# Performance work log

Hardware: AMD Instinct MI355X
Metric: run time of the kernel (lower is better)

The kernel has to match this reference:

```python
import jax, jax.numpy as jnp
import numpy as np

EMBED_DIM_LIST = [256, 512]
NUM_HEADS_LIST = [4, 8]
MAX_EMBED = 512
N_BASE = 8                       # = max(num_heads_list)
MAX_HS = max(EMBED_DIM_LIST) // min(NUM_HEADS_LIST)  # 128


def _config_masks():
    # One {0,1} mask per (emb, heads) config, shape [n_cfg, N_BASE, MAX_HS, MAX_EMBED].
    # Mask encodes: slice base weight [:head_size, :emb], zero-pad to (MAX_HS, MAX_EMBED),
    # and that only the first `heads` base heads receive a contribution.
    r = np.arange(MAX_HS)[:, None]
    c = np.arange(MAX_EMBED)[None, :]
    masks = []
    for emb in EMBED_DIM_LIST:
        for heads in NUM_HEADS_LIST:
            hs = emb // heads
            m2 = ((r < hs) & (c < emb)).astype(np.float32)      # [MAX_HS, MAX_EMBED]
            hm = (np.arange(N_BASE) < heads).astype(np.float32)  # [N_BASE]
            masks.append(hm[:, None, None] * m2[None])
    return jnp.asarray(np.stack(masks))  # [4, 8, 128, 512]

_CFG_MASKS = _config_masks()


def setup_inputs() -> dict:
    key = jax.random.key(0)
    k0, k1, k2, k3, k4 = jax.random.split(key, 5)
    B, T = 4, 2048
    x = jax.random.normal(k0, (B, T, MAX_EMBED), dtype=jnp.float32)
    weights = jax.random.uniform(k1, (len(EMBED_DIM_LIST) * len(NUM_HEADS_LIST),), dtype=jnp.float32)
    s = 0.02
    base_K = jax.random.normal(k2, (N_BASE, MAX_HS, MAX_EMBED), dtype=jnp.float32) * s
    base_Q = jax.random.normal(k3, (N_BASE, MAX_HS, MAX_EMBED), dtype=jnp.float32) * s
    base_V = jax.random.normal(k4, (N_BASE, MAX_HS, MAX_EMBED), dtype=jnp.float32) * s
    return {"x": x, "weights": weights, "base_K": base_K, "base_Q": base_Q, "base_V": base_V}


def reference(x, weights, base_K, base_Q, base_V):
    B, T, C = x.shape
    # Weight mixing: sum_i weights[i] * (padded slice of base weight) for each base head.
    eff = jnp.einsum('i,ihde->hde', weights, _CFG_MASKS)  # [H, MAX_HS, MAX_EMBED]
    Wk = eff * base_K
    Wq = eff * base_Q
    Wv = eff * base_V
    # Projections for all base heads at once: F.linear(x, W) == x @ W.T
    k = jnp.einsum('btc,hdc->bhtd', x, Wk)
    q = jnp.einsum('btc,hdc->bhtd', x, Wq)
    v = jnp.einsum('btc,hdc->bhtd', x, Wv)
    # Causal self-attention; scale uses k.shape[-1] == MAX_HS (padded head size), as in source.
    scale = 1.0 / jnp.sqrt(jnp.asarray(MAX_HS, dtype=x.dtype))
    att = jnp.einsum('bhtd,bhsd->bhts', q, k) * scale       # [B, H, T, T]
    tril = jnp.tril(jnp.ones((T, T), dtype=bool))
    att = jnp.where(tril, att, -jnp.inf)
    wei = jax.nn.softmax(att, axis=-1)                       # dropout = identity (eval)
    out = jnp.einsum('bhts,bhsd->bhtd', wei, v)              # [B, H, T, MAX_HS]
    # torch.cat(head_out_list, dim=-1) in head order == transpose + reshape
    return out.transpose(0, 2, 1, 3).reshape(B, T, N_BASE * MAX_HS)
```

## Files before the change

kernel.cpp:

```cpp
#include <hip/hip_runtime.h>
#include <hip/hip_bf16.h>
#include <stdint.h>

typedef __attribute__((ext_vector_type(8))) short bf16x8;
typedef __attribute__((ext_vector_type(4))) float f32x4;
typedef __attribute__((ext_vector_type(16))) float f32x16;

#define MFMA16(a,b,c) __builtin_amdgcn_mfma_f32_16x16x32_bf16((a),(b),(c),0,0,0)
#define MFMA32(a,b,c) __builtin_amdgcn_mfma_f32_32x32x16_bf16((a),(b),(c),0,0,0)
#define AS1 __attribute__((address_space(1)))
#define AS3 __attribute__((address_space(3)))

__device__ inline short f2bf(float f) {
    union { __hip_bfloat16 h; short s; } u;
    u.h = __float2bfloat16(f);
    return u.s;
}
__device__ inline uint32_t pack_bf16(float a, float b) {
    union { __hip_bfloat16 h; uint16_t u; } ua, ub;
    ua.h = __float2bfloat16(a); ub.h = __float2bfloat16(b);
    return (uint32_t)ua.u | ((uint32_t)ub.u << 16);
}

#if __has_builtin(__builtin_amdgcn_permlane32_swap)
#define SWAP32(x, y, a, b) { auto _r = __builtin_amdgcn_permlane32_swap((a),(b),false,false); \
                             (x) = _r[0]; (y) = _r[1]; }
#else
#define SWAP32(x, y, a, b) { uint32_t _ta = __shfl_xor((uint32_t)(a),32); \
                             uint32_t _tb = __shfl_xor((uint32_t)(b),32); \
                             (x) = hh_ ? _tb : (a); (y) = hh_ ? (b) : _ta; }
#endif

#define QSCALE 0.12751879523879295f

#define NW (8*128*512)
#define NX4 (8192*512/4)

__global__ void prep_kernel(const float* __restrict__ x,
                            const float* __restrict__ w,
                            const float* __restrict__ bK,
                            const float* __restrict__ bQ,
                            const float* __restrict__ bV,
                            short* __restrict__ xb,
                            short* __restrict__ W)
{
    const float w0 = w[0], w1 = w[1], w2 = w[2], w3 = w[3];
    for (int i = blockIdx.x * blockDim.x + threadIdx.x; i < NW + NX4;
         i += gridDim.x * blockDim.x) {
        if (i < NW) {
            int e = i & 511;
            int d = (i >> 9) & 127;
            int h = i >> 16;
            float eff = 0.f;
            if (h < 4) { eff += w2; if (d < 64 && e < 256) eff += w0; }
            if (d < 32 && e < 256) eff += w1;
            if (d < 64) eff += w3;
            W[i]          = f2bf(eff * bK[i]);
            W[i + NW]     = f2bf(eff * bQ[i] * QSCALE);
            W[i + 2*NW]   = f2bf(eff * bV[i]);
        } else {
            int j = i - NW;
            float4 v = ((const float4*)x)[j];
            short4 o;
            o.x = f2bf(v.x); o.y = f2bf(v.y); o.z = f2bf(v.z); o.w = f2bf(v.w);
            ((short4*)xb)[j] = o;
        }
    }
}

__global__ __launch_bounds__(256)
void proj_gemm(const short* __restrict__ A,
               const short* __restrict__ Bw,
               short* __restrict__ qkv)
{
    __shared__ short S[128 * 128];
    short* As = S;
    short* Bs = S + 128 * 64;
    const int tid = threadIdx.x;
    const int lane = tid & 63;
    const int wave = tid >> 6;
    const int wr = wave >> 1, wc = wave & 1;
    const int l15 = lane & 15, lk = lane >> 4;

    const int wg = (blockIdx.x & 7) * 192 + (blockIdx.x >> 3);
    const int bm = (wg / 24) * 128;
    const int bn = (wg % 24) * 128;

    char* Ab = (char*)As;
    char* Bb = (char*)Bs;
    char* Sb = (char*)S;
    f32x4 acc[4][4] = {};

    for (int k0 = 0; k0 < 512; k0 += 64) {
        __syncthreads();
#pragma unroll
        for (int i = 0; i < 4; ++i) {
            int c = i * 256 + tid;
            int lin = c * 16;
            int row = lin >> 7;
            int cof = ((lin & 127) ^ ((row & 7) << 4)) >> 1;
            __builtin_amdgcn_global_load_lds(
                (const AS1 void*)(A + (size_t)(bm + row) * 512 + k0 + cof),
                (AS3 void*)(As + c * 8), 16, 0, 0);
            __builtin_amdgcn_global_load_lds(
                (const AS1 void*)(Bw + (size_t)(bn + row) * 512 + k0 + cof),
                (AS3 void*)(Bs + c * 8), 16, 0, 0);
        }
        __syncthreads();
#pragma unroll
        for (int kk = 0; kk < 2; ++kk) {
            bf16x8 af[4], bfv[4];
#pragma unroll
            for (int mi = 0; mi < 4; ++mi) {
                int row = wr * 64 + mi * 16 + l15;
                af[mi] = *(const bf16x8*)(Ab + ((row * 128 + kk * 64 + lk * 16) ^ ((row & 7) << 4)));
            }
#pragma unroll
            for (int ni = 0; ni < 4; ++ni) {
                int row = wc * 64 + ni * 16 + l15;
                bfv[ni] = *(const bf16x8*)(Bb + ((row * 128 + kk * 64 + lk * 16) ^ ((row & 7) << 4)));
            }
#pragma unroll
            for (int mi = 0; mi < 4; ++mi)
#pragma unroll
                for (int ni = 0; ni < 4; ++ni)
                    acc[mi][ni] = MFMA16(af[mi], bfv[ni], acc[mi][ni]);
        }
    }

    const int proj = bn >> 10;
    const int b = bm >> 11;
    const int bh = b * 8 + ((bn & 1023) >> 7);
    const int tbase = bm & 2047;

    __syncthreads();
    if (proj == 2) {
#pragma unroll
        for (int mi = 0; mi < 4; ++mi) {
#pragma unroll
            for (int ni = 0; ni < 4; ++ni) {
                int dl = wc * 64 + ni * 16 + l15;
                int tlb = wr * 64 + mi * 16 + lk * 4;
                int byte0 = (dl * 256 + tlb * 2) ^ ((dl & 7) << 4);
                *(uint32_t*)(Sb + byte0)     = pack_bf16(acc[mi][ni][0], acc[mi][ni][1]);
                *(uint32_t*)(Sb + byte0 + 4) = pack_bf16(acc[mi][ni][2], acc[mi][ni][3]);
            }
        }
    } else {
#pragma unroll
        for (int mi = 0; mi < 4; ++mi) {
#pragma unroll
            for (int ni = 0; ni < 4; ++ni) {
                int dl = wc * 64 + ni * 16 + l15;
#pragma unroll
                for (int r = 0; r < 4; ++r) {
                    int tl = wr * 64 + mi * 16 + lk * 4 + r;
                    *(short*)(Sb + ((tl * 256 + dl * 2) ^ ((tl & 7) << 4))) = f2bf(acc[mi][ni][r]);
                }
            }
        }
    }
    __syncthreads();

    short* dst;
    if (proj == 2)
        dst = qkv + (size_t)2 * (32 * 2048 * 128) + (size_t)bh * 128 * 2048;
    else
        dst = qkv + (size_t)proj * (32 * 2048 * 128) + (size_t)bh * 2048 * 128;

#pragma unroll
    for (int i = 0; i < 8; ++i) {
        int c = i * 256 + tid;
        int row = c >> 4;
        uint4 v = *(const uint4*)(Sb + row * 256 + (((c & 15) * 16) ^ ((row & 7) << 4)));
        if (proj == 2) {
            *(uint4*)(dst + (size_t)row * 2048 + tbase + (c & 15) * 8) = v;
        } else {
            *(uint4*)(dst + (size_t)(tbase + row) * 128 + (c & 15) * 8) = v;
        }
    }
}

__device__ inline void stage_tile(const short* __restrict__ Kp,
                                  const short* __restrict__ Vp,
                                  char* smem, int buf)
{
    short* kls = (short*)(smem + (buf << 14));
    short* vls = (short*)(smem + 32768 + (buf << 14));
    const int tid = threadIdx.x;
#pragma unroll
    for (int i = 0; i < 4; ++i) {
        int c = i * 256 + tid;
        int lin = c * 16;
        int rk = lin >> 8;
        int kof = ((lin & 255) ^ ((rk & 15) << 4)) >> 1;
        __builtin_amdgcn_global_load_lds(
            (const AS1 void*)(Kp + (size_t)rk * 128 + kof),
            (AS3 void*)(kls + c * 8), 16, 0, 0);
        int rv = lin >> 8;
        int p = (lin & 255) ^ ((rv & 15) << 4);
        int d = rv * 2 + (p >> 7);
        int t = (p & 127) >> 1;
        __builtin_amdgcn_global_load_lds(
            (const AS1 void*)(Vp + (size_t)d * 2048 + t),
            (AS3 void*)(vls + c * 8), 16, 0, 0);
    }
}

__global__ __launch_bounds__(256, 2)
void attn_kernel(const short* __restrict__ qkv, float* __restrict__ out)
{
    extern __shared__ char smem[];
    const int tid = threadIdx.x, lane = tid & 63, wave = tid >> 6;
    const int l31 = lane & 31;
    const int hh_ = lane >> 5;

    const int bh = blockIdx.x & 31;
    const int half = blockIdx.x >> 8;
    const int idx = (blockIdx.x >> 5) & 7;
    const int qt = half ? idx : (15 - idx);
    const int q0 = qt * 128;

    const size_t HSTRIDE = (size_t)2048 * 128;
    const short* Kp = qkv + (size_t)bh * HSTRIDE;
    const short* Qp = qkv + (size_t)32 * HSTRIDE + (size_t)bh * HSTRIDE;
    const short* Vp = qkv + (size_t)64 * HSTRIDE + (size_t)bh * 128 * 2048;

    bf16x8 qf[8];
    {
        const short* qrow = Qp + (size_t)(q0 + wave * 32 + l31) * 128 + hh_ * 8;
#pragma unroll
        for (int dblk = 0; dblk < 8; ++dblk)
            qf[dblk] = *(const bf16x8*)(qrow + dblk * 16);
    }

    float mrow = -1e30f, lrow = 0.f;
    f32x16 acco[4] = {};

    const int ntiles = qt * 2 + 2;
    const int qwave = q0 + wave * 32;
    const int qglob = qwave + l31;

    stage_tile(Kp, Vp, smem, 0);
    int cur = 0;

    for (int jt = 0; jt < ntiles; ++jt) {
        const int j0 = jt * 64;
        __builtin_amdgcn_s_barrier();
        if (jt + 1 < ntiles) {
            stage_tile(Kp + (size_t)(j0 + 64) * 128, Vp + (j0 + 64),
                       smem, cur ^ 1);
            asm volatile("s_waitcnt vmcnt(8)" ::: "memory");
        } else {
            asm volatile("s_waitcnt vmcnt(0)" ::: "memory");
        }
        __builtin_amdgcn_sched_barrier(0);
        __builtin_amdgcn_s_barrier();
        __builtin_amdgcn_sched_barrier(0);

        if (j0 <= qwave + 31) {
            char* Kb = smem + (cur << 14);
            char* Vb = smem + 32768 + (cur << 14);

            f32x16 sacc[2] = {};
            __builtin_amdgcn_s_setprio(1);
#pragma unroll
            for (int dblk = 0; dblk < 8; ++dblk) {
#pragma unroll
                for (int kvt = 0; kvt < 2; ++kvt) {
                    int row = kvt * 32 + l31;
                    bf16x8 kf = *(const bf16x8*)(Kb + ((row * 256 + dblk * 32 + hh_ * 16) ^ ((row & 15) << 4)));
                    sacc[kvt] = MFMA32(kf, qf[dblk], sacc[kvt]);
                }
            }
            __builtin_amdgcn_s_setprio(0);

            if (j0 + 63 > qwave) {
#pragma unroll
                for (int kvt = 0; kvt < 2; ++kvt)
#pragma unroll
                    for (int r = 0; r < 16; ++r) {
                        int kvglob = j0 + kvt * 32 + (r & 3) + 8 * (r >> 2) + 4 * hh_;
                        if (kvglob > qglob) sacc[kvt][r] = -1e30f;
                    }
            }

            float pmax = -1e30f;
#pragma unroll
            for (int kvt = 0; kvt < 2; ++kvt)
#pragma unroll
                for (int r = 0; r < 16; r += 4) {
                    float a = fmaxf(sacc[kvt][r], sacc[kvt][r + 1]);
                    float b2 = fmaxf(sacc[kvt][r + 2], sacc[kvt][r + 3]);
                    pmax = fmaxf(pmax, fmaxf(a, b2));
                }
            pmax = fmaxf(pmax, __shfl_xor(pmax, 32));

            if (!__all(pmax - mrow <= 11.5416f)) {
                float mn = fmaxf(mrow, pmax);
                float alpha = __builtin_amdgcn_exp2f(mrow - mn);
                mrow = mn;
                lrow *= alpha;
#pragma unroll
                for (int r = 0; r < 16; ++r) {
                    float ar = __shfl(alpha, (r & 3) + 8 * (r >> 2) + 4 * hh_);
#pragma unroll
                    for (int dt = 0; dt < 4; ++dt) acco[dt][r] *= ar;
                }
            }

            float psum = 0.f;
            uint32_t pkA[2][4], pkB[2][4];
#pragma unroll
            for (int kvt = 0; kvt < 2; ++kvt) {
#pragma unroll
                for (int s = 0; s < 4; ++s) {
                    float p0 = __builtin_amdgcn_exp2f(sacc[kvt][4 * s + 0] - mrow);
                    float p1 = __builtin_amdgcn_exp2f(sacc[kvt][4 * s + 1] - mrow);
                    float p2 = __builtin_amdgcn_exp2f(sacc[kvt][4 * s + 2] - mrow);
                    float p3 = __builtin_amdgcn_exp2f(sacc[kvt][4 * s + 3] - mrow);
                    psum += (p0 + p1) + (p2 + p3);
                    pkA[kvt][s] = pack_bf16(p0, p1);
                    pkB[kvt][s] = pack_bf16(p2, p3);
                }
            }
            psum += __shfl_xor(psum, 32);
            lrow += psum;

            __builtin_amdgcn_s_setprio(1);
#pragma unroll
            for (int kb = 0; kb < 4; ++kb) {
                const int kvt = kb >> 1, kbl = kb & 1;
                uint32_t r0, r1, r2, r3;
                SWAP32(r0, r2, pkA[kvt][2 * kbl], pkA[kvt][2 * kbl + 1]);
                SWAP32(r1, r3, pkB[kvt][2 * kbl], pkB[kvt][2 * kbl + 1]);
                union { uint32_t u[4]; bf16x8 v; } pa;
                pa.u[0] = r0; pa.u[1] = r1; pa.u[2] = r2; pa.u[3] = r3;
#pragma unroll
                for (int dt = 0; dt < 4; ++dt) {
                    int d = dt * 32 + l31;
                    int r = d >> 1;
                    int inner = ((d & 1) << 7) + kb * 32 + hh_ * 16;
                    bf16x8 vf = *(const bf16x8*)(Vb + (r * 256 + (inner ^ ((r & 15) << 4))));
                    acco[dt] = MFMA32(pa.v, vf, acco[dt]);
                }
            }
            __builtin_amdgcn_s_setprio(0);
        }

        cur ^= 1;
    }

    float linv = 1.f / lrow;
    const int b = bh >> 3, hd = bh & 7;
#pragma unroll
    for (int r = 0; r < 16; ++r) {
        int ql = (r & 3) + 8 * (r >> 2) + 4 * hh_;
        float li = __shfl(linv, ql);
        int t = qwave + ql;
        float* o = out + (size_t)(b * 2048 + t) * 1024 + hd * 128 + l31;
#pragma unroll
        for (int dt = 0; dt < 4; ++dt)
            o[dt * 32] = acco[dt][r] * li;
    }
}

extern "C" void kernel_launch(void* const* d_in, const int* in_sizes, int n_in,
                              void* d_out, int out_size, void* d_ws, size_t ws_size,
                              hipStream_t stream) {
    const float* x  = (const float*)d_in[0];
    const float* w  = (const float*)d_in[1];
    const float* bK = (const float*)d_in[2];
    const float* bQ = (const float*)d_in[3];
    const float* bV = (const float*)d_in[4];

    short* xb  = (short*)d_ws;
    short* W   = (short*)((char*)d_ws + 8388608);
    short* qkv = (short*)((char*)d_ws + 8388608 + 3145728);
    float* out = (float*)d_out;

    hipFuncSetAttribute((const void*)attn_kernel,
                        hipFuncAttributeMaxDynamicSharedMemorySize, 65536);

    prep_kernel<<<2048, 256, 0, stream>>>(x, w, bK, bQ, bV, xb, W);
    proj_gemm<<<64 * 24, 256, 0, stream>>>(xb, W, qkv);
    attn_kernel<<<16 * 32, 256, 65536, stream>>>(qkv, out);
}
```

Measured before the change: 106.2 us.

## Split KV tile across wave pairs with 64-row query tiles and LDS merge

Shrinks the attention query tile from 128 to 64 rows and doubles the grid, launching the longest tiles first. Within each block, two wave pairs each own half of every 64-key tile and keep separate softmax states. The states are merged through LDS at the end. The aim is more blocks to balance the causal triangle across CUs and less idle time per wave. The cost is K/V staged twice as often per query row, and an extra LDS reduction with barriers.

Result: no change. 106.6 us (+0.4%).

```diff
diff --git a/kernel.cpp b/kernel.cpp
--- a/kernel.cpp
+++ b/kernel.cpp
@@ -216,10 +216,12 @@
     const int hh_ = lane >> 5;
 
     const int bh = blockIdx.x & 31;
-    const int half = blockIdx.x >> 8;
-    const int idx = (blockIdx.x >> 5) & 7;
-    const int qt = half ? idx : (15 - idx);
-    const int q0 = qt * 128;
+    const int s = 31 - (blockIdx.x >> 5);
+    const int q0 = s * 64;
+
+    const int qw = wave & 1;
+    const int kvh = wave >> 1;
+    const int kvoff = kvh * 32;
 
     const size_t HSTRIDE = (size_t)2048 * 128;
     const short* Kp = qkv + (size_t)bh * HSTRIDE;
@@ -228,7 +230,7 @@
 
     bf16x8 qf[8];
     {
-        const short* qrow = Qp + (size_t)(q0 + wave * 32 + l31) * 128 + hh_ * 8;
+        const short* qrow = Qp + (size_t)(q0 + qw * 32 + l31) * 128 + hh_ * 8;
 #pragma unroll
         for (int dblk = 0; dblk < 8; ++dblk)
             qf[dblk] = *(const bf16x8*)(qrow + dblk * 16);
@@ -237,8 +239,8 @@
     float mrow = -1e30f, lrow = 0.f;
     f32x16 acco[4] = {};
 
-    const int ntiles = qt * 2 + 2;
-    const int qwave = q0 + wave * 32;
+    const int ntiles = s + 1;
+    const int qwave = q0 + qw * 32;
     const int qglob = qwave + l31;
 
     stage_tile(Kp, Vp, smem, 0);
@@ -258,42 +260,36 @@
         __builtin_amdgcn_s_barrier();
         __builtin_amdgcn_sched_barrier(0);
 
-        if (j0 <= qwave + 31) {
+        const int kv0 = j0 + kvoff;
+        if (kv0 <= qwave + 31) {
             char* Kb = smem + (cur << 14);
             char* Vb = smem + 32768 + (cur << 14);
 
-            f32x16 sacc[2] = {};
+            f32x16 sacc = {};
             __builtin_amdgcn_s_setprio(1);
 #pragma unroll
             for (int dblk = 0; dblk < 8; ++dblk) {
-#pragma unroll
-                for (int kvt = 0; kvt < 2; ++kvt) {
-                    int row = kvt * 32 + l31;
-                    bf16x8 kf = *(const bf16x8*)(Kb + ((row * 256 + dblk * 32 + hh_ * 16) ^ ((row & 15) << 4)));
-                    sacc[kvt] = MFMA32(kf, qf[dblk], sacc[kvt]);
+                int row = kvoff + l31;
+                bf16x8 kf = *(const bf16x8*)(Kb + ((row * 256 + dblk * 32 + hh_ * 16) ^ ((row & 15) << 4)));
+                sacc = MFMA32(kf, qf[dblk], sacc);
+            }
+            __builtin_amdgcn_s_setprio(0);
+
+            if (kv0 + 31 > qwave) {
+#pragma unroll
+                for (int r = 0; r < 16; ++r) {
+                    int kvglob = kv0 + (r & 3) + 8 * (r >> 2) + 4 * hh_;
+                    if (kvglob > qglob) sacc[r] = -1e30f;
                 }
             }
-            __builtin_amdgcn_s_setprio(0);
-
-            if (j0 + 63 > qwave) {
-#pragma unroll
-                for (int kvt = 0; kvt < 2; ++kvt)
-#pragma unroll
-                    for (int r = 0; r < 16; ++r) {
-                        int kvglob = j0 + kvt * 32 + (r & 3) + 8 * (r >> 2) + 4 * hh_;
-                        if (kvglob > qglob) sacc[kvt][r] = -1e30f;
-                    }
-            }
 
             float pmax = -1e30f;
 #pragma unroll
-            for (int kvt = 0; kvt < 2; ++kvt)
-#pragma unroll
-                for (int r = 0; r < 16; r += 4) {
-                    float a = fmaxf(sacc[kvt][r], sacc[kvt][r + 1]);
-                    float b2 = fmaxf(sacc[kvt][r + 2], sacc[kvt][r + 3]);
-                    pmax = fmaxf(pmax, fmaxf(a, b2));
-                }
+            for (int r = 0; r < 16; r += 4) {
+                float a = fmaxf(sacc[r], sacc[r + 1]);
+                float b2 = fmaxf(sacc[r + 2], sacc[r + 3]);
+                pmax = fmaxf(pmax, fmaxf(a, b2));
+            }
             pmax = fmaxf(pmax, __shfl_xor(pmax, 32));
 
             if (!__all(pmax - mrow <= 11.5416f)) {
@@ -310,32 +306,29 @@
             }
 
             float psum = 0.f;
-            uint32_t pkA[2][4], pkB[2][4];
-#pragma unroll
-            for (int kvt = 0; kvt < 2; ++kvt) {
-#pragma unroll
-                for (int s = 0; s < 4; ++s) {
-                    float p0 = __builtin_amdgcn_exp2f(sacc[kvt][4 * s + 0] - mrow);
-                    float p1 = __builtin_amdgcn_exp2f(sacc[kvt][4 * s + 1] - mrow);
-                    float p2 = __builtin_amdgcn_exp2f(sacc[kvt][4 * s + 2] - mrow);
-                    float p3 = __builtin_amdgcn_exp2f(sacc[kvt][4 * s + 3] - mrow);
-                    psum += (p0 + p1) + (p2 + p3);
-                    pkA[kvt][s] = pack_bf16(p0, p1);
-                    pkB[kvt][s] = pack_bf16(p2, p3);
-                }
+            uint32_t pkA[4], pkB[4];
+#pragma unroll
+            for (int sg = 0; sg < 4; ++sg) {
+                float p0 = __builtin_amdgcn_exp2f(sacc[4 * sg + 0] - mrow);
+                float p1 = __builtin_amdgcn_exp2f(sacc[4 * sg + 1] - mrow);
+                float p2 = __builtin_amdgcn_exp2f(sacc[4 * sg + 2] - mrow);
+                float p3 = __builtin_amdgcn_exp2f(sacc[4 * sg + 3] - mrow);
+                psum += (p0 + p1) + (p2 + p3);
+                pkA[sg] = pack_bf16(p0, p1);
+                pkB[sg] = pack_bf16(p2, p3);
             }
             psum += __shfl_xor(psum, 32);
             lrow += psum;
 
             __builtin_amdgcn_s_setprio(1);
 #pragma unroll
-            for (int kb = 0; kb < 4; ++kb) {
-                const int kvt = kb >> 1, kbl = kb & 1;
+            for (int kbl = 0; kbl < 2; ++kbl) {
                 uint32_t r0, r1, r2, r3;
-                SWAP32(r0, r2, pkA[kvt][2 * kbl], pkA[kvt][2 * kbl + 1]);
-                SWAP32(r1, r3, pkB[kvt][2 * kbl], pkB[kvt][2 * kbl + 1]);
+                SWAP32(r0, r2, pkA[2 * kbl], pkA[2 * kbl + 1]);
+                SWAP32(r1, r3, pkB[2 * kbl], pkB[2 * kbl + 1]);
                 union { uint32_t u[4]; bf16x8 v; } pa;
                 pa.u[0] = r0; pa.u[1] = r1; pa.u[2] = r2; pa.u[3] = r3;
+                const int kb = kvh * 2 + kbl;
 #pragma unroll
                 for (int dt = 0; dt < 4; ++dt) {
                     int d = dt * 32 + l31;
@@ -351,17 +344,41 @@
         cur ^= 1;
     }
 
-    float linv = 1.f / lrow;
-    const int b = bh >> 3, hd = bh & 7;
-#pragma unroll
-    for (int r = 0; r < 16; ++r) {
-        int ql = (r & 3) + 8 * (r >> 2) + 4 * hh_;
-        float li = __shfl(linv, ql);
-        int t = qwave + ql;
-        float* o = out + (size_t)(b * 2048 + t) * 1024 + hd * 128 + l31;
+    __syncthreads();
+    float* ex = (float*)smem;
+    float* ml = (float*)(smem + 32768);
+    if (kvh == 1) {
+        float* dst = ex + qw * 4096;
 #pragma unroll
         for (int dt = 0; dt < 4; ++dt)
-            o[dt * 32] = acco[dt][r] * li;
+#pragma unroll
+            for (int r = 0; r < 16; ++r)
+                dst[(dt * 16 + r) * 64 + lane] = acco[dt][r];
+        ml[qw * 128 + lane * 2 + 0] = mrow;
+        ml[qw * 128 + lane * 2 + 1] = lrow;
+    }
+    __syncthreads();
+    if (kvh == 0) {
+        float m1 = ml[qw * 128 + lane * 2 + 0];
+        float l1 = ml[qw * 128 + lane * 2 + 1];
+        float M  = fmaxf(mrow, m1);
+        float a  = __builtin_amdgcn_exp2f(mrow - M);
+        float b2 = __builtin_amdgcn_exp2f(m1 - M);
+        float lf = lrow * a + l1 * b2;
+        float sA = a / lf, sB = b2 / lf;
+        const float* src = ex + qw * 4096;
+        const int b = bh >> 3, hd = bh & 7;
+#pragma unroll
+        for (int r = 0; r < 16; ++r) {
+            int ql = (r & 3) + 8 * (r >> 2) + 4 * hh_;
+            float sa = __shfl(sA, ql);
+            float sb = __shfl(sB, ql);
+            int t = qwave + ql;
+            float* o = out + (size_t)(b * 2048 + t) * 1024 + hd * 128 + l31;
+#pragma unroll
+            for (int dt = 0; dt < 4; ++dt)
+                o[dt * 32] = acco[dt][r] * sa + src[(dt * 16 + r) * 64 + lane] * sb;
+        }
     }
 }
 
@@ -384,5 +401,5 @@
 
     prep_kernel<<<2048, 256, 0, stream>>>(x, w, bK, bQ, bV, xb, W);
     proj_gemm<<<64 * 24, 256, 0, stream>>>(xb, W, qkv);
-    attn_kernel<<<16 * 32, 256, 65536, stream>>>(qkv, out);
-}
+    attn_kernel<<<32 * 32, 256, 65536, stream>>>(qkv, out);
+}
```
